# Kernel tuning notes

Hardware: AMD Instinct MI355X
Metric: run time of the kernel (lower is better)

## Reference

```python
import jax, jax.numpy as jnp
import numpy as np

RADIUS = float(1.5 * 6 * 0.025 / 2.0)  # filter_extent / 2 = 0.1125
N_FLUID, N_BOX, K_F, K_B = 16000, 8000, 64, 32
KS = 4  # kernel size per axis -> 64 bins
EPS = 1e-12


def _radius_neighbors(q, p, radius, K, exclude_self=False):
    Nq = q.shape[0]
    idx = np.zeros((Nq, K), np.int32)
    mask = np.zeros((Nq, K), bool)
    r2 = radius * radius
    kth = min(K, p.shape[0] - 1)
    for s in range(0, Nq, 2048):
        e = min(s + 2048, Nq)
        d2 = ((q[s:e, None, :] - p[None, :, :]) ** 2).sum(-1)
        if exclude_self:
            d2[np.arange(e - s), np.arange(s, e)] = np.inf
        part = np.argpartition(d2, kth, axis=1)[:, :K].astype(np.int32)
        dk = np.take_along_axis(d2, part, 1)
        m = dk <= r2
        part[~m] = 0
        idx[s:e] = part
        mask[s:e] = m
    return idx, mask


def ball_to_cube(d):
    """Volume-preserving map unit ball -> unit cube [-1,1]^3 (Open3D ball_to_cube_volume_preserving)."""
    x, y, z = d[..., 0], d[..., 1], d[..., 2]
    sq = x * x + y * y + z * z
    norm = jnp.sqrt(sq)
    # --- sphere -> cylinder (radius 1, height 2) ---
    xy_sq = x * x + y * y
    polar = (1.25 * z * z) > xy_sq
    s_pol = jnp.sqrt(3.0 * norm / (norm + jnp.abs(z) + EPS))
    s_eq = norm / jnp.sqrt(xy_sq + EPS)
    s = jnp.where(polar, s_pol, s_eq)
    xc = x * s
    yc = y * s
    zc = jnp.where(polar, jnp.sign(z) * norm, 1.5 * z)
    zero = sq < EPS
    xc = jnp.where(zero, 0.0, xc)
    yc = jnp.where(zero, 0.0, yc)
    zc = jnp.where(zero, 0.0, zc)
    # --- cylinder -> cube: inverse Shirley-Chiu concentric map on the xy disc ---
    rxy = jnp.sqrt(xc * xc + yc * yc)
    xbig = jnp.abs(xc) >= jnp.abs(yc)
    safe_x = jnp.where(jnp.abs(xc) > EPS, xc, 1.0)
    safe_y = jnp.where(jnp.abs(yc) > EPS, yc, 1.0)
    four_over_pi = 4.0 / np.pi
    u1 = jnp.sign(xc) * rxy
    v1 = u1 * four_over_pi * jnp.arctan(yc / safe_x)
    v2 = jnp.sign(yc) * rxy
    u2 = v2 * four_over_pi * jnp.arctan(xc / safe_y)
    u = jnp.where(xbig, u1, u2)
    v = jnp.where(xbig, v1, v2)
    zero_xy = rxy < EPS
    u = jnp.where(zero_xy, 0.0, u)
    v = jnp.where(zero_xy, 0.0, v)
    return jnp.stack([u, v, zc], axis=-1)


def cconv(feat_src, pos_src, pos_q, nbr_idx, nbr_mask, filt, bias):
    """ContinuousConv: trilinear (align_corners=True) filter interpolation, poly6 window, no normalization."""
    N = pos_q.shape[0]
    kz, ky, kx, cin, cout = filt.shape
    pj = pos_src[nbr_idx]                       # [N,K,3]
    fj = feat_src[nbr_idx]                      # [N,K,Cin]
    d = (pj - pos_q[:, None, :]) / RADIUS       # normalized offsets in unit ball
    r_sqr = jnp.sum(d * d, axis=-1)             # [N,K]
    win = jnp.clip((1.0 - r_sqr) ** 3, 0.0, 1.0) * nbr_mask.astype(fj.dtype)
    u = ball_to_cube(d)                         # [N,K,3] in [-1,1]
    ks = jnp.asarray([kx, ky, kz], d.dtype)
    g = (u * 0.5 + 0.5) * (ks - 1.0)            # align_corners=True grid coords
    i0 = jnp.clip(jnp.floor(g), 0.0, ks - 2.0).astype(jnp.int32)  # [N,K,3]
    t = g - i0                                  # trilinear fractions
    Fflat = filt.reshape(kz * ky * kx, cin, cout)
    A = jnp.zeros((N, kz * ky * kx, cin), fj.dtype)   # per-query bin accumulator
    n_idx = jnp.arange(N)[:, None]
    for dz in (0, 1):
        for dy in (0, 1):
            for dx in (0, 1):
                w = ((t[..., 0] if dx else 1.0 - t[..., 0])
                     * (t[..., 1] if dy else 1.0 - t[..., 1])
                     * (t[..., 2] if dz else 1.0 - t[..., 2])) * win
                bins = ((i0[..., 2] + dz) * ky + (i0[..., 1] + dy)) * kx + (i0[..., 0] + dx)
                A = A.at[n_idx, bins].add(w[..., None] * fj)
    return jnp.einsum('nbc,bco->no', A, Fflat) + bias


def _forward(pos, vel, box, box_feats,
             w_conv0_fluid, b_conv0_fluid, w_conv0_obstacle, b_conv0_obstacle,
             w_dense0, b_dense0, w_conv1, b_conv1, w_dense1, b_dense1,
             w_conv2, b_conv2, w_dense2, b_dense2,
             nbr_fluid_idx, nbr_fluid_mask, nbr_box_idx, nbr_box_mask):
    fluid_feats = jnp.concatenate([jnp.ones_like(pos[:, :1]), vel], axis=-1)  # [N,4]
    a_cf = cconv(fluid_feats, pos, pos, nbr_fluid_idx, nbr_fluid_mask, w_conv0_fluid, b_conv0_fluid)
    a_df = fluid_feats @ w_dense0 + b_dense0
    a_co = cconv(box_feats, box, pos, nbr_box_idx, nbr_box_mask, w_conv0_obstacle, b_conv0_obstacle)
    feats = jnp.concatenate([a_co, a_cf, a_df], axis=-1)                      # [N,96]
    inp1 = jax.nn.relu(feats)
    ans1 = cconv(inp1, pos, pos, nbr_fluid_idx, nbr_fluid_mask, w_conv1, b_conv1) + inp1 @ w_dense1 + b_dense1
    inp2 = jax.nn.relu(ans1)
    ans2 = (cconv(inp2, pos, pos, nbr_fluid_idx, nbr_fluid_mask, w_conv2, b_conv2)
            + inp2 @ w_dense2 + b_dense2 + ans1)                               # residual (64==64)
    return ans2  # particle_feat = ans_convs[-2] returned by forward()


def setup_inputs() -> dict:
    rng = np.random.default_rng(0)
    L = 1.357  # cube side chosen so avg neighbor count within RADIUS is ~48
    pos = rng.uniform(0, L, (N_FLUID, 3)).astype(np.float32)
    box = rng.uniform(0, L, (N_BOX, 3)).astype(np.float32)
    vel = (0.5 * rng.standard_normal((N_FLUID, 3))).astype(np.float32)
    nrm = rng.standard_normal((N_BOX, 3)).astype(np.float32)
    box_feats = nrm / np.linalg.norm(nrm, axis=-1, keepdims=True)
    nf_idx, nf_mask = _radius_neighbors(pos, pos, RADIUS, K_F, exclude_self=True)
    nb_idx, nb_mask = _radius_neighbors(pos, box, RADIUS, K_B, exclude_self=False)

    def filt(cin, cout):
        s = (6.0 / (cin * KS ** 3 + cout)) ** 0.5
        return (s * rng.standard_normal((KS, KS, KS, cin, cout))).astype(np.float32)

    def lin(cin, cout):
        s = (6.0 / (cin + cout)) ** 0.5
        return (s * rng.standard_normal((cin, cout))).astype(np.float32)

    z = lambda c: np.zeros((c,), np.float32)
    inp = dict(
        pos=pos, vel=vel, box=box, box_feats=box_feats,
        w_conv0_fluid=filt(4, 32), b_conv0_fluid=z(32),
        w_conv0_obstacle=filt(3, 32), b_conv0_obstacle=z(32),
        w_dense0=lin(4, 32), b_dense0=z(32),
        w_conv1=filt(96, 64), b_conv1=z(64), w_dense1=lin(96, 64), b_dense1=z(64),
        w_conv2=filt(64, 64), b_conv2=z(64), w_dense2=lin(64, 64), b_dense2=z(64),
        nbr_fluid_idx=nf_idx, nbr_fluid_mask=nf_mask,
        nbr_box_idx=nb_idx, nbr_box_mask=nb_mask,
    )
    return {k: jnp.asarray(v) for k, v in inp.items()}


def reference(pos, vel, box, box_feats,
              w_conv0_fluid, b_conv0_fluid, w_conv0_obstacle, b_conv0_obstacle,
              w_dense0, b_dense0, w_conv1, b_conv1, w_dense1, b_dense1,
              w_conv2, b_conv2, w_dense2, b_dense2,
              nbr_fluid_idx, nbr_fluid_mask, nbr_box_idx, nbr_box_mask):
    return _forward(pos, vel, box, box_feats,
                    w_conv0_fluid, b_conv0_fluid, w_conv0_obstacle, b_conv0_obstacle,
                    w_dense0, b_dense0, w_conv1, b_conv1, w_dense1, b_dense1,
                    w_conv2, b_conv2, w_dense2, b_dense2,
                    nbr_fluid_idx, nbr_fluid_mask, nbr_box_idx, nbr_box_mask)
```

## Files before the change

### kernel.cpp

```cpp
#include <hip/hip_runtime.h>
#include <cstdint>

#define DEVFN __device__ __forceinline__
#define AS1 __attribute__((address_space(1)))
#define AS3 __attribute__((address_space(3)))

using hh8 = __attribute__((ext_vector_type(8))) _Float16;
using f4  = __attribute__((ext_vector_type(4))) float;

constexpr float RAD  = 0.1125f;
constexpr float R2C  = RAD * RAD;
constexpr float EPSF = 1e-12f;
constexpr float FOPI = 1.27323954473516268615f;

DEVFN float sgnf(float a){ return (a > 0.f) ? 1.f : ((a < 0.f) ? -1.f : 0.f); }

DEVFN unsigned short f2h(float f){
  _Float16 h = (_Float16)f;
  union { _Float16 h; unsigned short u; } x; x.h = h; return x.u;
}
DEVFN hh8 ld_hh8(const unsigned short* p){ return *(const hh8*)p; }
DEVFN hh8 ld_b64x2(const unsigned short* p){
  union { unsigned long long q[2]; hh8 v; } u;
  u.q[0] = *(const unsigned long long*)(p);
  u.q[1] = *(const unsigned long long*)(p + 4);
  return u.v;
}
DEVFN void gld16(const void* g, void* l){
  __builtin_amdgcn_global_load_lds((const AS1 void*)g, (AS3 void*)l, 16, 0, 0);
}

DEVFN void nbr_geom(float ddx, float ddy, float ddz, float factor, int* bins, float* w8)
{
  float x = ddx / RAD, y = ddy / RAD, z = ddz / RAD;
  float sq = x*x + y*y + z*z;
  float omr = 1.f - sq;
  float win = (omr > 0.f) ? omr*omr*omr : 0.f;
  win *= factor;
  float nrm   = sqrtf(sq);
  float xy_sq = x*x + y*y;
  bool  polar = (1.25f*z*z) > xy_sq;
  float s = polar ? sqrtf(3.f*nrm/(nrm + fabsf(z) + EPSF))
                  : (nrm / sqrtf(xy_sq + EPSF));
  float xc = x*s, yc = y*s;
  float zc = polar ? (sgnf(z)*nrm) : (1.5f*z);
  if (sq < EPSF){ xc = 0.f; yc = 0.f; zc = 0.f; }
  float rxy  = sqrtf(xc*xc + yc*yc);
  bool  xbig = fabsf(xc) >= fabsf(yc);
  float sx = (fabsf(xc) > EPSF) ? xc : 1.f;
  float sy = (fabsf(yc) > EPSF) ? yc : 1.f;
  float u1 = sgnf(xc)*rxy;
  float v1 = u1 * FOPI * atanf(yc / sx);
  float v2 = sgnf(yc)*rxy;
  float u2 = v2 * FOPI * atanf(xc / sy);
  float u = xbig ? u1 : u2;
  float v = xbig ? v1 : v2;
  if (rxy < EPSF){ u = 0.f; v = 0.f; }
  float gx = (u *0.5f + 0.5f)*3.f;
  float gy = (v *0.5f + 0.5f)*3.f;
  float gz = (zc*0.5f + 0.5f)*3.f;
  float fx = fminf(fmaxf(floorf(gx), 0.f), 2.f);
  float fy = fminf(fmaxf(floorf(gy), 0.f), 2.f);
  float fz = fminf(fmaxf(floorf(gz), 0.f), 2.f);
  int ix = (int)fx, iy = (int)fy, iz = (int)fz;
  float tx = gx - fx, ty = gy - fy, tz = gz - fz;
  float wx[2] = {1.f - tx, tx};
  float wy[2] = {1.f - ty, ty};
  float wz[2] = {1.f - tz, tz};
  #pragma unroll
  for (int dz2 = 0; dz2 < 2; ++dz2)
    #pragma unroll
    for (int dy2 = 0; dy2 < 2; ++dy2)
      #pragma unroll
      for (int dx2 = 0; dx2 < 2; ++dx2){
        int c = (dz2 << 2) | (dy2 << 1) | dx2;
        bins[c] = ((iz + dz2)*4 + (iy + dy2))*4 + (ix + dx2);
        w8[c]   = wx[dx2]*wy[dy2]*wz[dz2]*win;
      }
}

__global__ __launch_bounds__(256)
void k0_scatter(const float* __restrict__ pos, const float* __restrict__ vel,
                const float* __restrict__ box, const float* __restrict__ boxf,
                const int* __restrict__ nfi, const int* __restrict__ nbi,
                int KB, unsigned short* __restrict__ Abuf)
{
  const int n = blockIdx.x, t = threadIdx.x;
  const int lane = t & 63, w = t >> 6, r = lane & 15, h = lane >> 4;

  __shared__ __align__(16) unsigned short LWf[64*64];
  __shared__ __align__(16) unsigned short LWo[64*32];
  __shared__ __align__(16) unsigned short LBf[16*64];
  __shared__ __align__(16) unsigned short LBo[16*32];
  __shared__ __align__(16) unsigned short Aout[512];
  __shared__ int gjf[64]; __shared__ int gjo[32];

  const float qx = pos[3*n], qy = pos[3*n+1], qz = pos[3*n+2];
  int bins[8]; float w8[8];

  if (w == 0){
    const int k = lane;
    const int j = nfi[(size_t)n*64 + k];
    const float ddx = pos[3*j] - qx, ddy = pos[3*j+1] - qy, ddz = pos[3*j+2] - qz;
    const float d2 = ddx*ddx + ddy*ddy + ddz*ddz;
    unsigned long long zm = __ballot(j == 0);
    int fz = __ffsll(zm) - 1;
    float factor = (j != 0) ? 1.f : ((k == fz && d2 <= R2C && n != 0) ? 1.f : 0.f);
    nbr_geom(ddx, ddy, ddz, factor, bins, w8);
    gjf[k] = j;
  } else if (w == 1){
    const int k = lane;
    const bool act = k < KB;
    const int j = act ? nbi[(size_t)n*KB + k] : 1;
    float ddx = 0.f, ddy = 0.f, ddz = 0.f, d2 = 1e30f;
    if (act){
      ddx = box[3*j] - qx; ddy = box[3*j+1] - qy; ddz = box[3*j+2] - qz;
      d2 = ddx*ddx + ddy*ddy + ddz*ddz;
    }
    unsigned long long zm = __ballot(act && j == 0);
    int fz = __ffsll(zm) - 1;
    float factor = (j != 0) ? 1.f : ((k == fz && d2 <= R2C) ? 1.f : 0.f);
    nbr_geom(ddx, ddy, ddz, factor, bins, w8);
    if (act) gjo[k] = j;
  } else {
    int4 z4 = make_int4(0,0,0,0);
    for (int i = t-128; i < 512; i += 128) *(int4*)&LWf[i*8] = z4;
    for (int i = t-128; i < 256; i += 128) *(int4*)&LWo[i*8] = z4;
    if (t-128 < 128) *(int4*)&LBf[(t-128)*8] = z4;
    if (t-128 <  64) *(int4*)&LBo[(t-128)*8] = z4;
  }
  __syncthreads();

  if (w == 0){
    #pragma unroll
    for (int q = 0; q < 8; ++q){
      int b = bins[q];
      LWf[b*64 + (lane ^ ((b&7)<<3))] = f2h(w8[q]);
    }
  } else if (w == 1){
    if (lane < KB){
      #pragma unroll
      for (int q = 0; q < 8; ++q){
        int b = bins[q];
        LWo[b*32 + (lane ^ ((b&3)<<3))] = f2h(w8[q]);
      }
    }
  } else if (w == 2){
    const int k = lane; const int j = gjf[k];
    LBf[0*64 + k] = f2h(1.f);
    LBf[1*64 + (k ^ 8)]  = f2h(vel[3*j]);
    LBf[2*64 + (k ^ 16)] = f2h(vel[3*j+1]);
    LBf[3*64 + (k ^ 24)] = f2h(vel[3*j+2]);
  } else {
    if (lane < KB){
      const int k = lane; const int j = gjo[k];
      LBo[0*32 + k]        = f2h(boxf[3*j]);
      LBo[1*32 + (k ^ 8)]  = f2h(boxf[3*j+1]);
      LBo[2*32 + (k ^ 16)] = f2h(boxf[3*j+2]);
    }
  }
  __syncthreads();

  f4 aF = {0.f,0.f,0.f,0.f}, aO = {0.f,0.f,0.f,0.f};
  {
    const int b = 16*w + r;
    #pragma unroll
    for (int ks = 0; ks < 2; ++ks){
      hh8 a  = ld_hh8(&LWf[b*64 + (((ks*4+h) ^ (b&7))<<3)]);
      hh8 bb = ld_hh8(&LBf[r*64 + (((ks*4+h) ^ (r&7))<<3)]);
      aF = __builtin_amdgcn_mfma_f32_16x16x32_f16(a, bb, aF, 0,0,0);
    }
    hh8 a2 = ld_hh8(&LWo[b*32 + ((h ^ (b&3))<<3)]);
    hh8 b2 = ld_hh8(&LBo[r*32 + ((h ^ (r&3))<<3)]);
    aO = __builtin_amdgcn_mfma_f32_16x16x32_f16(a2, b2, aO, 0,0,0);
  }
  #pragma unroll
  for (int rr = 0; rr < 4; ++rr){
    int b2 = 16*w + h*4 + rr;
    if (r < 4) Aout[b2*4 + r]       = f2h(aF[rr]);
    if (r < 3) Aout[256 + b2*3 + r] = f2h(aO[rr]);
  }
  if (t == 0){ Aout[448] = f2h(1.f); Aout[452] = f2h(1.f); }
  if (t < 3)   Aout[449 + t] = f2h(vel[3*n + t]);
  if (t < 59)  Aout[453 + t] = 0;
  __syncthreads();

  const int key = n & 7;
  if (t < 64){
    int4 v = *(const int4*)&Aout[t*8];
    *(int4*)&Abuf[(size_t)n*512 + (size_t)(t ^ key)*8] = v;
  }
}

template<int C>
__global__ __launch_bounds__(256)
void k1_scatter(const float* __restrict__ pos, const unsigned short* __restrict__ feat,
                const int* __restrict__ nfi, int n0, unsigned short* __restrict__ Abuf)
{
  constexpr int BST  = (C == 96) ? 100 : 68;
  constexpr int Kpad = (C == 96) ? 6528 : 4416;
  constexpr int CT = C/16;
  constexpr int BTS = 68;
  const int nloc = blockIdx.x;
  const int n = n0 + nloc;
  const int t = threadIdx.x;
  const int lane = t & 63, w = t >> 6, r = lane & 15, h = lane >> 4;

  __shared__ __align__(16) unsigned short sh[4096 + C*BTS];
  unsigned short* W  = sh;
  unsigned short* BT = sh + 4096;
  __shared__ int gj[64];

  int jreg = 0; float qx=0.f,qy=0.f,qz=0.f,px=0.f,py=0.f,pz=0.f;
  if (w == 0){
    jreg = nfi[(size_t)n*64 + lane];
    gj[lane] = jreg;
    qx = pos[3*n]; qy = pos[3*n+1]; qz = pos[3*n+2];
    px = pos[3*jreg]; py = pos[3*jreg+1]; pz = pos[3*jreg+2];
  } else {
    int4 z4 = make_int4(0,0,0,0);
    for (int i = t - 64; i < 512; i += 192) *(int4*)&W[i*8] = z4;
  }
  __syncthreads();

  if (w == 0){
    const int k = lane;
    const float ddx = px - qx, ddy = py - qy, ddz = pz - qz;
    const float d2 = ddx*ddx + ddy*ddy + ddz*ddz;
    unsigned long long zm = __ballot(jreg == 0);
    int fz = __ffsll(zm) - 1;
    float factor = (jreg != 0) ? 1.f : ((k == fz && d2 <= R2C && n != 0) ? 1.f : 0.f);
    int bins[8]; float w8[8];
    nbr_geom(ddx, ddy, ddz, factor, bins, w8);
    #pragma unroll
    for (int q = 0; q < 8; ++q){
      int b = bins[q];
      W[b*64 + (lane ^ ((b&7)<<3))] = f2h(w8[q]);
    }
  } else {
    const int tt = t - 64;
    if constexpr (C == 96){
      const int kb = tt / 48;
      const int cp = tt - kb*48;
      const int c0 = cp*2;
      unsigned short* b0 = BT + c0*BTS;
      unsigned short* b1 = BT + (c0+1)*BTS;
      #pragma unroll 4
      for (int pass = 0; pass < 16; ++pass){
        const int k = pass*4 + kb;
        const int j = gj[k];
        const uint32_t v = *(const uint32_t*)(feat + (size_t)j*96 + c0);
        b0[k] = (unsigned short)(v & 0xffffu);
        b1[k] = (unsigned short)(v >> 16);
      }
    } else {
      const int kb = tt >> 5;
      const int cp = tt & 31;
      const int c0 = cp*2;
      unsigned short* b0 = BT + c0*BTS;
      unsigned short* b1 = BT + (c0+1)*BTS;
      #pragma unroll 4
      for (int pass = 0; pass < 11; ++pass){
        const int k = pass*6 + kb;
        if (k < 64){
          const int j = gj[k];
          const uint32_t v = *(const uint32_t*)(feat + (size_t)j*64 + c0);
          b0[k] = (unsigned short)(v & 0xffffu);
          b1[k] = (unsigned short)(v >> 16);
        }
      }
    }
  }
  __syncthreads();

  f4 acc[CT];
  #pragma unroll
  for (int ct = 0; ct < CT; ++ct) acc[ct] = f4{0.f,0.f,0.f,0.f};
  const int b = 16*w + r;
  #pragma unroll
  for (int ks = 0; ks < 2; ++ks){
    hh8 a = ld_hh8(&W[b*64 + (((ks*4+h) ^ (b&7))<<3)]);
    const int kc = (ks*4 + h)*8;
    #pragma unroll
    for (int ct = 0; ct < CT; ++ct){
      int c = ct*16 + r;
      hh8 bb = ld_b64x2(&BT[c*BTS + kc]);
      acc[ct] = __builtin_amdgcn_mfma_f32_16x16x32_f16(bb, a, acc[ct], 0,0,0);
    }
  }
  __syncthreads();

  unsigned short* Aout = sh;
  #pragma unroll
  for (int ct = 0; ct < CT; ++ct){
    unsigned long long pk =
        (unsigned long long)f2h(acc[ct][0])
      | ((unsigned long long)f2h(acc[ct][1]) << 16)
      | ((unsigned long long)f2h(acc[ct][2]) << 32)
      | ((unsigned long long)f2h(acc[ct][3]) << 48);
    const int c0 = ct*16 + h*4;
    *(unsigned long long*)&Aout[b*BST + c0] = pk;
  }
  Aout[(t >> 2)*BST + C + (t & 3)] = 0;
  if constexpr (C == 96){
    if (t < 32) Aout[6496 + t] = 0;
  }
  if (t < C) Aout[64*BST + t] = feat[(size_t)n*C + t];
  __syncthreads();

  const int key = nloc & 7;
  const size_t rowBase = (size_t)nloc * Kpad;
  for (int ch = t; ch < Kpad/8; ch += 256){
    int4 v = *(const int4*)&Aout[ch*8];
    *(int4*)&Abuf[rowBase + (size_t)(ch ^ key)*8] = v;
  }
}

__global__ __launch_bounds__(256)
void k_bpack(const float* __restrict__ F, const float* __restrict__ Wd,
             int Cin, int BST, int Cd, int Kpad, unsigned short* __restrict__ BpkT)
{
  int idx = blockIdx.x*256 + threadIdx.x;
  int chunks = Kpad/8;
  if (idx >= 64*chunks) return;
  int o = idx / chunks, ch = idx - o*chunks;
  const int kDense = 64*BST;
  union { int4 v; unsigned short u[8]; } pk;
  #pragma unroll
  for (int e = 0; e < 8; ++e){
    int kp = ch*8 + e;
    float f = 0.f;
    if (kp < kDense){
      int bin = kp / BST, c = kp - bin*BST;
      if (c < Cin) f = F[((size_t)bin*Cin + c)*64 + o];
    } else if (kp < kDense + Cd){
      f = Wd[(size_t)(kp - kDense)*64 + o];
    }
    pk.u[e] = f2h(f);
  }
  *(int4*)&BpkT[((size_t)o*chunks + (ch ^ (o&7)))*8] = pk.v;
}

__global__ __launch_bounds__(256)
void k_bpack0(const float* __restrict__ Wfilt, const float* __restrict__ Ofilt,
              const float* __restrict__ Wd0, const float* __restrict__ bco,
              const float* __restrict__ bcf, const float* __restrict__ bd0,
              unsigned short* __restrict__ Bpk0)
{
  int idx = blockIdx.x*256 + threadIdx.x;
  if (idx >= 96*64) return;
  int o = idx >> 6, ch = idx & 63;
  union { int4 v; unsigned short u[8]; } pk;
  #pragma unroll
  for (int e = 0; e < 8; ++e){
    int kp = ch*8 + e;
    float f = 0.f;
    if (kp < 256){
      if (o >= 32 && o < 64) f = Wfilt[(size_t)kp*32 + (o - 32)];
    } else if (kp < 448){
      if (o < 32)            f = Ofilt[(size_t)(kp - 256)*32 + o];
    } else if (kp < 452){
      if (o >= 64)           f = Wd0[(size_t)(kp - 448)*32 + (o - 64)];
    } else if (kp == 452){
      f = (o < 32) ? bco[o] : (o < 64) ? bcf[o - 32] : bd0[o - 64];
    }
    pk.u[e] = f2h(f);
  }
  *(int4*)&Bpk0[((size_t)o*64 + (ch ^ (o&7)))*8] = pk.v;
}

template<int NT>
__global__ __launch_bounds__(256)
void k2_gemm(const unsigned short* __restrict__ Abuf, const unsigned short* __restrict__ BpkT,
             float* __restrict__ partial, int n0, int CHa, int Kpad, int ktot,
             int sB, int NF)
{
  const int t = threadIdx.x;
  const int lane = t & 63, w = t >> 6, r = lane & 15, h = lane >> 4;
  const int wbase = t & ~63;
  const int seg = blockIdx.y;
  const int ks0 = seg*sB;
  const int ks1 = (ks0 + sB < ktot) ? (ks0 + sB) : ktot;
  const int rowBase = blockIdx.x * 128;

  __shared__ __align__(16) unsigned short Asub[128*64];
  __shared__ __align__(16) unsigned short Bsub[16*NT*64];

  f4 acc[2][NT];
  #pragma unroll
  for (int i = 0; i < 2; ++i)
    #pragma unroll
    for (int j = 0; j < NT; ++j) acc[i][j] = f4{0.f,0.f,0.f,0.f};

  for (int ks = ks0; ks < ks1; ++ks){
    #pragma unroll
    for (int i = 0; i < 4; ++i){
      int lin = i*256 + t;
      int row = lin >> 3, lc = lin & 7;
      int grow = rowBase + row; if (grow >= CHa) grow = CHa - 1;
      gld16(&Abuf[(size_t)grow*Kpad + ks*64 + lc*8],
            &Asub[(size_t)(i*256 + wbase)*8]);
    }
    #pragma unroll
    for (int i = 0; i < NT/2; ++i){
      int lin = i*256 + t;
      int o = lin >> 3, lc = lin & 7;
      gld16(&BpkT[(size_t)o*Kpad + ks*64 + lc*8],
            &Bsub[(size_t)(i*256 + wbase)*8]);
    }
    __syncthreads();
    #pragma unroll
    for (int kh = 0; kh < 2; ++kh){
      hh8 a0 = ld_hh8(&Asub[(w*32 +      r)*64 + (((kh*4+h) ^ (r&7))<<3)]);
      hh8 a1 = ld_hh8(&Asub[(w*32 + 16 + r)*64 + (((kh*4+h) ^ (r&7))<<3)]);
      #pragma unroll
      for (int nt = 0; nt < NT; ++nt){
        hh8 bb = ld_hh8(&Bsub[(nt*16 + r)*64 + (((kh*4+h) ^ (r&7))<<3)]);
        acc[0][nt] = __builtin_amdgcn_mfma_f32_16x16x32_f16(a0, bb, acc[0][nt], 0,0,0);
        acc[1][nt] = __builtin_amdgcn_mfma_f32_16x16x32_f16(a1, bb, acc[1][nt], 0,0,0);
      }
    }
    __syncthreads();
  }

  #pragma unroll
  for (int mt = 0; mt < 2; ++mt)
    #pragma unroll
    for (int rr = 0; rr < 4; ++rr){
      int m = rowBase + w*32 + mt*16 + h*4 + rr;
      if (m < CHa){
        float* op = partial + ((size_t)seg*NF + n0 + m)*(16*NT);
        #pragma unroll
        for (int nt = 0; nt < NT; ++nt)
          op[nt*16 + r] = acc[mt][nt][rr];
      }
    }
}

__global__ __launch_bounds__(256)
void k_epi(const float* __restrict__ partial, const float* __restrict__ bc,
           const float* __restrict__ bd, const float* __restrict__ resid,
           float* __restrict__ outRaw, unsigned short* __restrict__ outRelu, int total)
{
  const int i = blockIdx.x*256 + threadIdx.x;
  if (i >= total) return;
  float v = 0.f;
  #pragma unroll
  for (int s = 0; s < 8; ++s) v += partial[(size_t)s*total + i];
  const int o = i & 63;
  v += bc[o] + bd[o];
  if (resid)   v += resid[i];
  if (outRaw)  outRaw[i]  = v;
  if (outRelu) outRelu[i] = f2h(fmaxf(v, 0.f));
}

__global__ __launch_bounds__(256)
void k_epi0(const float* __restrict__ partial, unsigned short* __restrict__ outRelu,
            int total)
{
  const int i = blockIdx.x*256 + threadIdx.x;
  if (i >= total) return;
  float v = 0.f;
  #pragma unroll
  for (int s = 0; s < 4; ++s) v += partial[(size_t)s*total + i];
  outRelu[i] = f2h(fmaxf(v, 0.f));
}

extern "C" void kernel_launch(void* const* d_in, const int* in_sizes, int n_in,
                              void* d_out, int out_size, void* d_ws, size_t ws_size,
                              hipStream_t stream)
{
  const float* pos  = (const float*)d_in[0];
  const float* vel  = (const float*)d_in[1];
  const float* box  = (const float*)d_in[2];
  const float* boxf = (const float*)d_in[3];
  const float* Wc0f = (const float*)d_in[4];
  const float* bc0f = (const float*)d_in[5];
  const float* Wc0o = (const float*)d_in[6];
  const float* bc0o = (const float*)d_in[7];
  const float* Wd0  = (const float*)d_in[8];
  const float* bd0  = (const float*)d_in[9];
  const float* Wc1  = (const float*)d_in[10];
  const float* bc1  = (const float*)d_in[11];
  const float* Wd1  = (const float*)d_in[12];
  const float* bd1  = (const float*)d_in[13];
  const float* Wc2  = (const float*)d_in[14];
  const float* bc2  = (const float*)d_in[15];
  const float* Wd2  = (const float*)d_in[16];
  const float* bd2  = (const float*)d_in[17];
  const int* nfi = (const int*)d_in[18];
  const int* nbi = (const int*)d_in[20];
  const int NF = in_sizes[0]/3;
  const int KB = in_sizes[20]/NF;
  float* out = (float*)d_out;

  const int Kp1 = 6528, Kp2 = 4416;

  char* wsb = (char*)d_ws;
  auto alloc = [&](size_t bytes){ char* p = wsb; wsb += (bytes + 255) & ~(size_t)255; return p; };
  unsigned short* inp1 = (unsigned short*)alloc((size_t)NF*96*2);
  float* ans1    = (float*)alloc((size_t)NF*64*4);
  unsigned short* inp2 = (unsigned short*)alloc((size_t)NF*64*2);
  float* partial = (float*)alloc((size_t)8*NF*64*4);
  unsigned short* Bpk1 = (unsigned short*)alloc((size_t)64*Kp1*2);
  unsigned short* Bpk2 = (unsigned short*)alloc((size_t)64*Kp2*2);
  unsigned short* Bpk0 = (unsigned short*)alloc((size_t)96*512*2);
  unsigned short* Abuf = (unsigned short*)wsb;
  size_t usedB = (size_t)(wsb - (char*)d_ws);
  size_t availUS = (ws_size > usedB) ? (ws_size - usedB)/2 : 0;

  auto chunkOf = [&](int Kpad)->int{
    long long c = (long long)(availUS / (size_t)Kpad);
    if (c >= NF) return NF;
    int ch = (int)c & ~127;
    if (ch < 128) ch = 128;
    return ch;
  };

  k_bpack0<<<(96*64 + 255)/256, 256, 0, stream>>>(Wc0f, Wc0o, Wd0, bc0o, bc0f, bd0, Bpk0);
  k_bpack<<<(64*(Kp1/8) + 255)/256, 256, 0, stream>>>(Wc1, Wd1, 96, 100, 96, Kp1, Bpk1);
  k_bpack<<<(64*(Kp2/8) + 255)/256, 256, 0, stream>>>(Wc2, Wd2, 64,  68, 64, Kp2, Bpk2);

  {
    k0_scatter<<<NF, 256, 0, stream>>>(pos, vel, box, boxf, nfi, nbi, KB, Abuf);
    int tiles = (NF + 127)/128;
    k2_gemm<6><<<dim3(tiles, 4), 256, 0, stream>>>(Abuf, Bpk0, partial, 0, NF,
                                                   512, 8, 2, NF);
    k_epi0<<<(NF*96 + 255)/256, 256, 0, stream>>>(partial, inp1, NF*96);
  }
  {
    int CH = chunkOf(Kp1);
    for (int n0 = 0; n0 < NF; n0 += CH){
      int CHa = (n0 + CH < NF) ? CH : (NF - n0);
      k1_scatter<96><<<CHa, 256, 0, stream>>>(pos, inp1, nfi, n0, Abuf);
      int tiles = (CHa + 127)/128;
      k2_gemm<4><<<dim3(tiles, 8), 256, 0, stream>>>(Abuf, Bpk1, partial, n0, CHa,
                                                     Kp1, Kp1/64, 13, NF);
    }
    k_epi<<<(NF*64 + 255)/256, 256, 0, stream>>>(partial, bc1, bd1, nullptr,
                                                 ans1, inp2, NF*64);
  }
  {
    int CH = chunkOf(Kp2);
    for (int n0 = 0; n0 < NF; n0 += CH){
      int CHa = (n0 + CH < NF) ? CH : (NF - n0);
      k1_scatter<64><<<CHa, 256, 0, stream>>>(pos, inp2, nfi, n0, Abuf);
      int tiles = (CHa + 127)/128;
      k2_gemm<4><<<dim3(tiles, 8), 256, 0, stream>>>(Abuf, Bpk2, partial, n0, CHa,
                                                     Kp2, Kp2/64, 9, NF);
    }
    k_epi<<<(NF*64 + 255)/256, 256, 0, stream>>>(partial, bc2, bd2, ans1,
                                                 out, nullptr, NF*64);
  }
}
```

Measured before the change: 250.8 us.

## Replace split-K GEMM plus epilogue kernels with small-tile fused-epilogue GEMM

```diff
diff --git a/kernel.cpp b/kernel.cpp
--- a/kernel.cpp
+++ b/kernel.cpp
@@ -371,38 +371,36 @@
 
 template<int NT>
 __global__ __launch_bounds__(256)
-void k2_gemm(const unsigned short* __restrict__ Abuf, const unsigned short* __restrict__ BpkT,
-             float* __restrict__ partial, int n0, int CHa, int Kpad, int ktot,
-             int sB, int NF)
-{
+void k3_gemm(const unsigned short* __restrict__ Abuf, const unsigned short* __restrict__ BpkT,
+             const float* __restrict__ bc, const float* __restrict__ bd,
+             const float* __restrict__ resid,
+             float* __restrict__ outF32, unsigned short* __restrict__ outH16,
+             int n0, int CHa, int Kpad)
+{
+  constexpr int NH = NT/2;
+  constexpr int BN = 16*NT;
   const int t = threadIdx.x;
   const int lane = t & 63, w = t >> 6, r = lane & 15, h = lane >> 4;
+  const int wm = w >> 1, wn = w & 1;
   const int wbase = t & ~63;
-  const int seg = blockIdx.y;
-  const int ks0 = seg*sB;
-  const int ks1 = (ks0 + sB < ktot) ? (ks0 + sB) : ktot;
-  const int rowBase = blockIdx.x * 128;
-
-  __shared__ __align__(16) unsigned short Asub[128*64];
+  const int locBase = blockIdx.x * 32;
+  const int ktot = Kpad >> 6;
+
+  __shared__ __align__(16) unsigned short Asub[32*64];
   __shared__ __align__(16) unsigned short Bsub[16*NT*64];
 
-  f4 acc[2][NT];
-  #pragma unroll
-  for (int i = 0; i < 2; ++i)
-    #pragma unroll
-    for (int j = 0; j < NT; ++j) acc[i][j] = f4{0.f,0.f,0.f,0.f};
-
-  for (int ks = ks0; ks < ks1; ++ks){
-    #pragma unroll
-    for (int i = 0; i < 4; ++i){
-      int lin = i*256 + t;
-      int row = lin >> 3, lc = lin & 7;
-      int grow = rowBase + row; if (grow >= CHa) grow = CHa - 1;
-      gld16(&Abuf[(size_t)grow*Kpad + ks*64 + lc*8],
-            &Asub[(size_t)(i*256 + wbase)*8]);
-    }
-    #pragma unroll
-    for (int i = 0; i < NT/2; ++i){
+  f4 acc[NH];
+  #pragma unroll
+  for (int i = 0; i < NH; ++i) acc[i] = f4{0.f,0.f,0.f,0.f};
+
+  int arow = t >> 3, alc = t & 7;
+  int grow = locBase + arow; if (grow >= CHa) grow = CHa - 1;
+  const unsigned short* aSrc = Abuf + (size_t)grow*Kpad + alc*8;
+
+  for (int ks = 0; ks < ktot; ++ks){
+    gld16(aSrc + ks*64, &Asub[(size_t)wbase*8]);
+    #pragma unroll
+    for (int i = 0; i < NH; ++i){
       int lin = i*256 + t;
       int o = lin >> 3, lc = lin & 7;
       gld16(&BpkT[(size_t)o*Kpad + ks*64 + lc*8],
@@ -411,59 +409,35 @@
     __syncthreads();
     #pragma unroll
     for (int kh = 0; kh < 2; ++kh){
-      hh8 a0 = ld_hh8(&Asub[(w*32 +      r)*64 + (((kh*4+h) ^ (r&7))<<3)]);
-      hh8 a1 = ld_hh8(&Asub[(w*32 + 16 + r)*64 + (((kh*4+h) ^ (r&7))<<3)]);
+      hh8 a = ld_hh8(&Asub[(wm*16 + r)*64 + (((kh*4+h) ^ (r&7))<<3)]);
       #pragma unroll
-      for (int nt = 0; nt < NT; ++nt){
-        hh8 bb = ld_hh8(&Bsub[(nt*16 + r)*64 + (((kh*4+h) ^ (r&7))<<3)]);
-        acc[0][nt] = __builtin_amdgcn_mfma_f32_16x16x32_f16(a0, bb, acc[0][nt], 0,0,0);
-        acc[1][nt] = __builtin_amdgcn_mfma_f32_16x16x32_f16(a1, bb, acc[1][nt], 0,0,0);
+      for (int nt = 0; nt < NH; ++nt){
+        int o = (wn*NH + nt)*16 + r;
+        hh8 bb = ld_hh8(&Bsub[o*64 + (((kh*4+h) ^ (r&7))<<3)]);
+        acc[nt] = __builtin_amdgcn_mfma_f32_16x16x32_f16(a, bb, acc[nt], 0,0,0);
       }
     }
     __syncthreads();
   }
 
   #pragma unroll
-  for (int mt = 0; mt < 2; ++mt)
+  for (int nt = 0; nt < NH; ++nt){
+    const int o = (wn*NH + nt)*16 + r;
+    float badd = 0.f;
+    if (bc) badd += bc[o];
+    if (bd) badd += bd[o];
     #pragma unroll
     for (int rr = 0; rr < 4; ++rr){
-      int m = rowBase + w*32 + mt*16 + h*4 + rr;
-      if (m < CHa){
-        float* op = partial + ((size_t)seg*NF + n0 + m)*(16*NT);
-        #pragma unroll
-        for (int nt = 0; nt < NT; ++nt)
-          op[nt*16 + r] = acc[mt][nt][rr];
+      const int lrow = locBase + wm*16 + h*4 + rr;
+      if (lrow < CHa){
+        const size_t m = (size_t)(n0 + lrow);
+        float v = acc[nt][rr] + badd;
+        if (resid)  v += resid[m*BN + o];
+        if (outF32) outF32[m*BN + o] = v;
+        if (outH16) outH16[m*BN + o] = f2h(fmaxf(v, 0.f));
       }
     }
-}
-
-__global__ __launch_bounds__(256)
-void k_epi(const float* __restrict__ partial, const float* __restrict__ bc,
-           const float* __restrict__ bd, const float* __restrict__ resid,
-           float* __restrict__ outRaw, unsigned short* __restrict__ outRelu, int total)
-{
-  const int i = blockIdx.x*256 + threadIdx.x;
-  if (i >= total) return;
-  float v = 0.f;
-  #pragma unroll
-  for (int s = 0; s < 8; ++s) v += partial[(size_t)s*total + i];
-  const int o = i & 63;
-  v += bc[o] + bd[o];
-  if (resid)   v += resid[i];
-  if (outRaw)  outRaw[i]  = v;
-  if (outRelu) outRelu[i] = f2h(fmaxf(v, 0.f));
-}
-
-__global__ __launch_bounds__(256)
-void k_epi0(const float* __restrict__ partial, unsigned short* __restrict__ outRelu,
-            int total)
-{
-  const int i = blockIdx.x*256 + threadIdx.x;
-  if (i >= total) return;
-  float v = 0.f;
-  #pragma unroll
-  for (int s = 0; s < 4; ++s) v += partial[(size_t)s*total + i];
-  outRelu[i] = f2h(fmaxf(v, 0.f));
+  }
 }
 
 extern "C" void kernel_launch(void* const* d_in, const int* in_sizes, int n_in,
@@ -501,7 +475,6 @@
   unsigned short* inp1 = (unsigned short*)alloc((size_t)NF*96*2);
   float* ans1    = (float*)alloc((size_t)NF*64*4);
   unsigned short* inp2 = (unsigned short*)alloc((size_t)NF*64*2);
-  float* partial = (float*)alloc((size_t)8*NF*64*4);
   unsigned short* Bpk1 = (unsigned short*)alloc((size_t)64*Kp1*2);
   unsigned short* Bpk2 = (unsigned short*)alloc((size_t)64*Kp2*2);
   unsigned short* Bpk0 = (unsigned short*)alloc((size_t)96*512*2);
@@ -523,33 +496,28 @@
 
   {
     k0_scatter<<<NF, 256, 0, stream>>>(pos, vel, box, boxf, nfi, nbi, KB, Abuf);
-    int tiles = (NF + 127)/128;
-    k2_gemm<6><<<dim3(tiles, 4), 256, 0, stream>>>(Abuf, Bpk0, partial, 0, NF,
-                                                   512, 8, 2, NF);
-    k_epi0<<<(NF*96 + 255)/256, 256, 0, stream>>>(partial, inp1, NF*96);
+    int tiles = (NF + 31)/32;
+    k3_gemm<6><<<tiles, 256, 0, stream>>>(Abuf, Bpk0, nullptr, nullptr, nullptr,
+                                          nullptr, inp1, 0, NF, 512);
   }
   {
     int CH = chunkOf(Kp1);
     for (int n0 = 0; n0 < NF; n0 += CH){
       int CHa = (n0 + CH < NF) ? CH : (NF - n0);
       k1_scatter<96><<<CHa, 256, 0, stream>>>(pos, inp1, nfi, n0, Abuf);
-      int tiles = (CHa + 127)/128;
-      k2_gemm<4><<<dim3(tiles, 8), 256, 0, stream>>>(Abuf, Bpk1, partial, n0, CHa,
-                                                     Kp1, Kp1/64, 13, NF);
-    }
-    k_epi<<<(NF*64 + 255)/256, 256, 0, stream>>>(partial, bc1, bd1, nullptr,
-                                                 ans1, inp2, NF*64);
+      int tiles = (CHa + 31)/32;
+      k3_gemm<4><<<tiles, 256, 0, stream>>>(Abuf, Bpk1, bc1, bd1, nullptr,
+                                            ans1, inp2, n0, CHa, Kp1);
+    }
   }
   {
     int CH = chunkOf(Kp2);
     for (int n0 = 0; n0 < NF; n0 += CH){
       int CHa = (n0 + CH < NF) ? CH : (NF - n0);
       k1_scatter<64><<<CHa, 256, 0, stream>>>(pos, inp2, nfi, n0, Abuf);
-      int tiles = (CHa + 127)/128;
-      k2_gemm<4><<<dim3(tiles, 8), 256, 0, stream>>>(Abuf, Bpk2, partial, n0, CHa,
-                                                     Kp2, Kp2/64, 9, NF);
-    }
-    k_epi<<<(NF*64 + 255)/256, 256, 0, stream>>>(partial, bc2, bd2, ans1,
-                                                 out, nullptr, NF*64);
-  }
-}
+      int tiles = (CHa + 31)/32;
+      k3_gemm<4><<<tiles, 256, 0, stream>>>(Abuf, Bpk2, bc2, bd2, ans1,
+                                            out, nullptr, n0, CHa, Kp2);
+    }
+  }
+}
```

Result: slower. 268.4 us (+7.0%).

## Replace split-K partial buffers with atomic accumulation and retile feature gather

Applied to the files above, without the earlier changes.

```diff
diff --git a/kernel.cpp b/kernel.cpp
--- a/kernel.cpp
+++ b/kernel.cpp
@@ -20,10 +20,12 @@
   union { _Float16 h; unsigned short u; } x; x.h = h; return x.u;
 }
 DEVFN hh8 ld_hh8(const unsigned short* p){ return *(const hh8*)p; }
-DEVFN hh8 ld_b64x2(const unsigned short* p){
-  union { unsigned long long q[2]; hh8 v; } u;
-  u.q[0] = *(const unsigned long long*)(p);
-  u.q[1] = *(const unsigned long long*)(p + 4);
+DEVFN hh8 ld_b32x4(const unsigned short* p){
+  union { unsigned int d[4]; hh8 v; } u;
+  u.d[0] = *(const unsigned int*)(p);
+  u.d[1] = *(const unsigned int*)(p + 2);
+  u.d[2] = *(const unsigned int*)(p + 4);
+  u.d[3] = *(const unsigned int*)(p + 6);
   return u.v;
 }
 DEVFN void gld16(const void* g, void* l){
@@ -200,7 +202,7 @@
   constexpr int BST  = (C == 96) ? 100 : 68;
   constexpr int Kpad = (C == 96) ? 6528 : 4416;
   constexpr int CT = C/16;
-  constexpr int BTS = 68;
+  constexpr int BTS = 66;
   const int nloc = blockIdx.x;
   const int n = n0 + nloc;
   const int t = threadIdx.x;
@@ -240,34 +242,22 @@
   } else {
     const int tt = t - 64;
     if constexpr (C == 96){
-      const int kb = tt / 48;
-      const int cp = tt - kb*48;
-      const int c0 = cp*2;
-      unsigned short* b0 = BT + c0*BTS;
-      unsigned short* b1 = BT + (c0+1)*BTS;
+      const int kb = (tt >= 96) ? 1 : 0;
+      const int c  = tt - 96*kb;
+      unsigned short* brow = BT + c*BTS;
       #pragma unroll 4
-      for (int pass = 0; pass < 16; ++pass){
-        const int k = pass*4 + kb;
-        const int j = gj[k];
-        const uint32_t v = *(const uint32_t*)(feat + (size_t)j*96 + c0);
-        b0[k] = (unsigned short)(v & 0xffffu);
-        b1[k] = (unsigned short)(v >> 16);
+      for (int pass = 0; pass < 32; ++pass){
+        const int k = pass*2 + kb;
+        brow[k] = feat[(size_t)gj[k]*96 + c];
       }
     } else {
-      const int kb = tt >> 5;
-      const int cp = tt & 31;
-      const int c0 = cp*2;
-      unsigned short* b0 = BT + c0*BTS;
-      unsigned short* b1 = BT + (c0+1)*BTS;
+      const int kb = tt >> 6;
+      const int c  = tt & 63;
+      unsigned short* brow = BT + c*BTS;
       #pragma unroll 4
-      for (int pass = 0; pass < 11; ++pass){
-        const int k = pass*6 + kb;
-        if (k < 64){
-          const int j = gj[k];
-          const uint32_t v = *(const uint32_t*)(feat + (size_t)j*64 + c0);
-          b0[k] = (unsigned short)(v & 0xffffu);
-          b1[k] = (unsigned short)(v >> 16);
-        }
+      for (int pass = 0; pass < 22; ++pass){
+        const int k = pass*3 + kb;
+        if (k < 64) brow[k] = feat[(size_t)gj[k]*64 + c];
       }
     }
   }
@@ -284,7 +274,7 @@
     #pragma unroll
     for (int ct = 0; ct < CT; ++ct){
       int c = ct*16 + r;
-      hh8 bb = ld_b64x2(&BT[c*BTS + kc]);
+      hh8 bb = ld_b32x4(&BT[c*BTS + kc]);
       acc[ct] = __builtin_amdgcn_mfma_f32_16x16x32_f16(bb, a, acc[ct], 0,0,0);
     }
   }
@@ -372,8 +362,8 @@
 template<int NT>
 __global__ __launch_bounds__(256)
 void k2_gemm(const unsigned short* __restrict__ Abuf, const unsigned short* __restrict__ BpkT,
-             float* __restrict__ partial, int n0, int CHa, int Kpad, int ktot,
-             int sB, int NF)
+             float* __restrict__ accum, int n0, int CHa, int Kpad, int ktot,
+             int sB)
 {
   const int t = threadIdx.x;
   const int lane = t & 63, w = t >> 6, r = lane & 15, h = lane >> 4;
@@ -429,41 +419,35 @@
     for (int rr = 0; rr < 4; ++rr){
       int m = rowBase + w*32 + mt*16 + h*4 + rr;
       if (m < CHa){
-        float* op = partial + ((size_t)seg*NF + n0 + m)*(16*NT);
+        float* op = accum + (size_t)(n0 + m)*(16*NT);
         #pragma unroll
         for (int nt = 0; nt < NT; ++nt)
-          op[nt*16 + r] = acc[mt][nt][rr];
+          unsafeAtomicAdd(op + nt*16 + r, acc[mt][nt][rr]);
       }
     }
 }
 
 __global__ __launch_bounds__(256)
-void k_epi(const float* __restrict__ partial, const float* __restrict__ bc,
+void k_epi(const float* __restrict__ accum, const float* __restrict__ bc,
            const float* __restrict__ bd, const float* __restrict__ resid,
            float* __restrict__ outRaw, unsigned short* __restrict__ outRelu, int total)
 {
   const int i = blockIdx.x*256 + threadIdx.x;
   if (i >= total) return;
-  float v = 0.f;
-  #pragma unroll
-  for (int s = 0; s < 8; ++s) v += partial[(size_t)s*total + i];
   const int o = i & 63;
-  v += bc[o] + bd[o];
+  float v = accum[i] + bc[o] + bd[o];
   if (resid)   v += resid[i];
   if (outRaw)  outRaw[i]  = v;
   if (outRelu) outRelu[i] = f2h(fmaxf(v, 0.f));
 }
 
 __global__ __launch_bounds__(256)
-void k_epi0(const float* __restrict__ partial, unsigned short* __restrict__ outRelu,
+void k_epi0(const float* __restrict__ accum, unsigned short* __restrict__ outRelu,
             int total)
 {
   const int i = blockIdx.x*256 + threadIdx.x;
   if (i >= total) return;
-  float v = 0.f;
-  #pragma unroll
-  for (int s = 0; s < 4; ++s) v += partial[(size_t)s*total + i];
-  outRelu[i] = f2h(fmaxf(v, 0.f));
+  outRelu[i] = f2h(fmaxf(accum[i], 0.f));
 }
 
 extern "C" void kernel_launch(void* const* d_in, const int* in_sizes, int n_in,
@@ -501,7 +485,7 @@
   unsigned short* inp1 = (unsigned short*)alloc((size_t)NF*96*2);
   float* ans1    = (float*)alloc((size_t)NF*64*4);
   unsigned short* inp2 = (unsigned short*)alloc((size_t)NF*64*2);
-  float* partial = (float*)alloc((size_t)8*NF*64*4);
+  float* accum   = (float*)alloc((size_t)NF*96*4);
   unsigned short* Bpk1 = (unsigned short*)alloc((size_t)64*Kp1*2);
   unsigned short* Bpk2 = (unsigned short*)alloc((size_t)64*Kp2*2);
   unsigned short* Bpk0 = (unsigned short*)alloc((size_t)96*512*2);
@@ -522,34 +506,37 @@
   k_bpack<<<(64*(Kp2/8) + 255)/256, 256, 0, stream>>>(Wc2, Wd2, 64,  68, 64, Kp2, Bpk2);
 
   {
+    hipMemsetAsync(accum, 0, (size_t)NF*96*4, stream);
     k0_scatter<<<NF, 256, 0, stream>>>(pos, vel, box, boxf, nfi, nbi, KB, Abuf);
     int tiles = (NF + 127)/128;
-    k2_gemm<6><<<dim3(tiles, 4), 256, 0, stream>>>(Abuf, Bpk0, partial, 0, NF,
-                                                   512, 8, 2, NF);
-    k_epi0<<<(NF*96 + 255)/256, 256, 0, stream>>>(partial, inp1, NF*96);
+    k2_gemm<6><<<dim3(tiles, 4), 256, 0, stream>>>(Abuf, Bpk0, accum, 0, NF,
+                                                   512, 8, 2);
+    k_epi0<<<(NF*96 + 255)/256, 256, 0, stream>>>(accum, inp1, NF*96);
   }
   {
+    hipMemsetAsync(accum, 0, (size_t)NF*64*4, stream);
     int CH = chunkOf(Kp1);
     for (int n0 = 0; n0 < NF; n0 += CH){
       int CHa = (n0 + CH < NF) ? CH : (NF - n0);
       k1_scatter<96><<<CHa, 256, 0, stream>>>(pos, inp1, nfi, n0, Abuf);
       int tiles = (CHa + 127)/128;
-      k2_gemm<4><<<dim3(tiles, 8), 256, 0, stream>>>(Abuf, Bpk1, partial, n0, CHa,
-                                                     Kp1, Kp1/64, 13, NF);
-    }
-    k_epi<<<(NF*64 + 255)/256, 256, 0, stream>>>(partial, bc1, bd1, nullptr,
+      k2_gemm<4><<<dim3(tiles, 8), 256, 0, stream>>>(Abuf, Bpk1, accum, n0, CHa,
+                                                     Kp1, Kp1/64, 13);
+    }
+    k_epi<<<(NF*64 + 255)/256, 256, 0, stream>>>(accum, bc1, bd1, nullptr,
                                                  ans1, inp2, NF*64);
   }
   {
+    hipMemsetAsync(accum, 0, (size_t)NF*64*4, stream);
     int CH = chunkOf(Kp2);
     for (int n0 = 0; n0 < NF; n0 += CH){
       int CHa = (n0 + CH < NF) ? CH : (NF - n0);
       k1_scatter<64><<<CHa, 256, 0, stream>>>(pos, inp2, nfi, n0, Abuf);
       int tiles = (CHa + 127)/128;
-      k2_gemm<4><<<dim3(tiles, 8), 256, 0, stream>>>(Abuf, Bpk2, partial, n0, CHa,
-                                                     Kp2, Kp2/64, 9, NF);
-    }
-    k_epi<<<(NF*64 + 255)/256, 256, 0, stream>>>(partial, bc2, bd2, ans1,
+      k2_gemm<4><<<dim3(tiles, 8), 256, 0, stream>>>(Abuf, Bpk2, accum, n0, CHa,
+                                                     Kp2, Kp2/64, 9);
+    }
+    k_epi<<<(NF*64 + 255)/256, 256, 0, stream>>>(accum, bc2, bd2, ans1,
                                                  out, nullptr, NF*64);
   }
 }
```

Result: slower. 319.1 us (+27.2%).
